# Kernel optimization log

Hardware: AMD Instinct MI355X
Metric: run time of the kernel (lower is better)

The kernel has to match this reference:

```python
import jax, jax.numpy as jnp
import numpy as np

B, T, S, A, H = 256, 256, 64, 16, 512  # batch, time, state_dim, action_dim, hypernet hidden


def setup_inputs() -> dict:
    key = jax.random.key(0)
    ks = jax.random.split(key, 12)
    x0 = jax.random.normal(ks[0], (B, S), dtype=jnp.float32)
    us = jax.random.normal(ks[1], (B, T, A), dtype=jnp.float32)
    # a_net: state_dim -> H -> S*S   (hypernetwork generating A(zx))
    Wa1 = jax.random.normal(ks[2], (S, H), dtype=jnp.float32) * 0.05
    ba1 = jax.random.normal(ks[3], (H,), dtype=jnp.float32) * 0.01
    Wa2 = jax.random.normal(ks[4], (H, S * S), dtype=jnp.float32) * 0.002  # small -> stable recurrence
    ba2 = jax.random.normal(ks[5], (S * S,), dtype=jnp.float32) * 0.002
    # b_net: action_dim -> H -> S*A  (hypernetwork generating B(zu))
    Wb1 = jax.random.normal(ks[6], (A, H), dtype=jnp.float32) * 0.05
    bb1 = jax.random.normal(ks[7], (H,), dtype=jnp.float32) * 0.01
    Wb2 = jax.random.normal(ks[8], (H, S * A), dtype=jnp.float32) * 0.02
    bb2 = jax.random.normal(ks[9], (S * A,), dtype=jnp.float32) * 0.02
    return {"x0": x0, "us": us, "Wa1": Wa1, "ba1": ba1, "Wa2": Wa2, "ba2": ba2,
            "Wb1": Wb1, "bb1": bb1, "Wb2": Wb2, "bb2": bb2}


def reference(x0, us, Wa1, ba1, Wa2, ba2, Wb1, bb1, Wb2, bb2):
    """HyperLinearSSM.rollout: x_{t+1} = A(x_t) @ x_t + B(u_t) @ u_t (zx=x, zu=u)."""
    def step(x, u):
        # hypernetwork-generated state matrix A(zx=x): [B, S, S]
        ha = jnp.tanh(x @ Wa1 + ba1)
        Amat = (ha @ Wa2 + ba2).reshape(-1, S, S)
        # hypernetwork-generated input matrix B(zu=u): [B, S, A]
        hb = jnp.tanh(u @ Wb1 + bb1)
        Bmat = (hb @ Wb2 + bb2).reshape(-1, S, A)
        x_next = jnp.einsum('bij,bj->bi', Amat, x) + jnp.einsum('bij,bj->bi', Bmat, u)
        return x_next, x_next

    us_t = jnp.transpose(us, (1, 0, 2))  # [T, B, A]
    _, xs = jax.lax.scan(step, x0, us_t)  # xs: [T, B, S]
    return jnp.transpose(xs, (1, 0, 2))   # [B, T, S]
```

## Files before the change

kernel.cpp:

```cpp
#include <hip/hip_runtime.h>

#define BSZ 256
#define TSZ 256
#define SSZ 64
#define ASZ 16
#define HSZ 512

typedef float f32x4 __attribute__((ext_vector_type(4)));
typedef short bf16x8 __attribute__((ext_vector_type(8)));
typedef unsigned short u16x8 __attribute__((ext_vector_type(8)));
typedef unsigned long long u64;
typedef unsigned short ushort_t;

#define XBUF_BYTES ((size_t)4 * BSZ * SSZ * sizeof(u64))
#define WT_ELEMS   ((size_t)4096 * 512)
#define WS_NEEDED  (XBUF_BYTES + 3 * WT_ELEMS * sizeof(ushort_t))


#define MF_X_OFF    0
#define MF_RED_OFF  4096
#define MF_HAH_OFF  4608
#define MF_HAM_OFF  (4608 + 16640)
#define MF_HAL_OFF  (21248 + 16640)
#define MF_WCH_OFF  (37888 + 16640)
#define MF_SMEM     (54528 + 2 * 3 * 16384)

#define NCH 16
#define HA_STR 20
#define X_OFF   0
#define HA_OFF  1024
#define W_OFF   (HA_OFF + HSZ * HA_STR)
#define RED_OFF (W_OFF + 3 * 32 * 256)
#define SMEM_FLOATS (RED_OFF + 512)
#define SMEM_BYTES  (SMEM_FLOATS * 4)

__device__ __forceinline__ void stage16(const void* gp, void* lp) {
    __builtin_amdgcn_global_load_lds(
        (const __attribute__((address_space(1))) void*)gp,
        (__attribute__((address_space(3))) void*)lp, 16, 0, 0);
}

__device__ __forceinline__ float wait_tag(const u64* p, unsigned tag) {
    u64 v = __hip_atomic_load(p, __ATOMIC_RELAXED, __HIP_MEMORY_SCOPE_AGENT);
    while ((unsigned)(v >> 32) != tag) {
        __builtin_amdgcn_s_sleep(1);
        v = __hip_atomic_load(p, __ATOMIC_RELAXED, __HIP_MEMORY_SCOPE_AGENT);
    }
    return __uint_as_float((unsigned)v);
}

__device__ __forceinline__ ushort_t f32_to_bf16(float f) {
    unsigned u = __float_as_uint(f);
    unsigned r = u + 0x7FFFu + ((u >> 16) & 1u);
    return (ushort_t)(r >> 16);
}
__device__ __forceinline__ float bf16_to_f32(ushort_t h) {
    return __uint_as_float((unsigned)h << 16);
}

__global__ __launch_bounds__(256) void wsplit_kernel(
    const float* __restrict__ Wa2,
    ushort_t* __restrict__ wth, ushort_t* __restrict__ wtm,
    ushort_t* __restrict__ wtl)
{
    __shared__ float tile[64][65];
    const int bc = blockIdx.x & 63;
    const int bh = blockIdx.x >> 6;
    const int c0 = bc * 64, h0 = bh * 64;
    const int tid = threadIdx.x;

    const int lr = tid >> 4, lc4 = (tid & 15) * 4;
    #pragma unroll
    for (int p = 0; p < 4; ++p) {
        const int h = p * 16 + lr;
        *(f32x4*)&tile[h][lc4] =
            *(const f32x4*)(Wa2 + (size_t)(h0 + h) * 4096 + c0 + lc4);
    }
    __syncthreads();

    const int col = tid >> 2, hb = (tid & 3) * 16;
    u16x8 H0, H1, M0, M1, L0, L1;
    #pragma unroll
    for (int q = 0; q < 16; ++q) {
        const float v = tile[hb + q][col];
        const ushort_t H = f32_to_bf16(v);
        const float r1 = v - bf16_to_f32(H);
        const ushort_t M = f32_to_bf16(r1);
        const ushort_t L = f32_to_bf16(r1 - bf16_to_f32(M));
        if (q < 8) { H0[q] = H; M0[q] = M; L0[q] = L; }
        else       { H1[q-8] = H; M1[q-8] = M; L1[q-8] = L; }
    }
    const int col_g = c0 + col;
    const int hbase = h0 + hb;
    const int kk    = hbase >> 5;
    const int sl0   = (hbase >> 3) & 3;
    const size_t atom0 = (((size_t)(col_g >> 5) * 16 + kk) * 4 + sl0) * 32
                       + (col_g & 31);
    const size_t atom1 = atom0 + 32;
    *(u16x8*)(wth + atom0 * 8) = H0;  *(u16x8*)(wth + atom1 * 8) = H1;
    *(u16x8*)(wtm + atom0 * 8) = M0;  *(u16x8*)(wtm + atom1 * 8) = M1;
    *(u16x8*)(wtl + atom0 * 8) = L0;  *(u16x8*)(wtl + atom1 * 8) = L1;
}

__global__ __launch_bounds__(256) void bu_kernel(
    const float* __restrict__ us,
    const float* __restrict__ Wb1, const float* __restrict__ bb1,
    const float* __restrict__ Wb2, const float* __restrict__ bb2,
    float* __restrict__ out)
{
    __shared__ float u_lds[16][16];
    __shared__ float hb_lds[16][HSZ + 4];

    const int tid = threadIdx.x;
    const long s0 = (long)blockIdx.x * 16;

    u_lds[tid >> 4][tid & 15] = us[s0 * ASZ + tid];
    __syncthreads();

    #pragma unroll
    for (int rep = 0; rep < 2; ++rep) {
        const int h = tid + rep * 256;
        float acc[16];
        const float b1 = bb1[h];
        #pragma unroll
        for (int s = 0; s < 16; ++s) acc[s] = b1;
        #pragma unroll
        for (int a = 0; a < ASZ; ++a) {
            const float w = Wb1[a * HSZ + h];
            #pragma unroll
            for (int s = 0; s < 16; ++s) acc[s] += u_lds[s][a] * w;
        }
        #pragma unroll
        for (int s = 0; s < 16; ++s) hb_lds[s][h] = tanhf(acc[s]);
    }
    __syncthreads();

    const int i  = tid & 63;
    const int sg = tid >> 6;

    float ur[4][ASZ];
    #pragma unroll
    for (int s4 = 0; s4 < 4; ++s4)
        #pragma unroll
        for (int a = 0; a < ASZ; ++a) ur[s4][a] = u_lds[sg * 4 + s4][a];

    float acc[4];
    {
        float wb[ASZ];
        const float4* bp = (const float4*)(bb2 + i * ASZ);
        #pragma unroll
        for (int q = 0; q < 4; ++q) {
            float4 v = bp[q];
            wb[q*4+0] = v.x; wb[q*4+1] = v.y; wb[q*4+2] = v.z; wb[q*4+3] = v.w;
        }
        #pragma unroll
        for (int s4 = 0; s4 < 4; ++s4) {
            float t = 0.f;
            #pragma unroll
            for (int a = 0; a < ASZ; ++a) t += wb[a] * ur[s4][a];
            acc[s4] = t;
        }
    }

    for (int h = 0; h < HSZ; ++h) {
        float w[ASZ];
        const float4* wp = (const float4*)(Wb2 + (size_t)h * (SSZ * ASZ) + i * ASZ);
        #pragma unroll
        for (int q = 0; q < 4; ++q) {
            float4 v = wp[q];
            w[q*4+0] = v.x; w[q*4+1] = v.y; w[q*4+2] = v.z; w[q*4+3] = v.w;
        }
        #pragma unroll
        for (int s4 = 0; s4 < 4; ++s4) {
            float t = 0.f;
            #pragma unroll
            for (int a = 0; a < ASZ; ++a) t += w[a] * ur[s4][a];
            acc[s4] += hb_lds[sg * 4 + s4][h] * t;
        }
    }

    #pragma unroll
    for (int s4 = 0; s4 < 4; ++s4)
        out[(s0 + sg * 4 + s4) * SSZ + i] = acc[s4];
}

__global__ __launch_bounds__(512, 1) void ssm_mfma(
    const float* __restrict__ x0,
    const float* __restrict__ Wa1, const float* __restrict__ ba1,
    const ushort_t* __restrict__ wth, const ushort_t* __restrict__ wtm,
    const ushort_t* __restrict__ wtl, const float* __restrict__ ba2,
    float* __restrict__ out, u64* __restrict__ xbuf)
{
    extern __shared__ char smem[];
    float* x_lds = (float*)(smem + MF_X_OFF);
    float* red   = (float*)(smem + MF_RED_OFF);
    char*  haH   = smem + MF_HAH_OFF;
    char*  haM   = smem + MF_HAM_OFF;
    char*  haL   = smem + MF_HAL_OFF;
    char*  wch   = smem + MF_WCH_OFF;

    const int tid  = threadIdx.x;
    const int lane = tid & 63;
    const int wv   = tid >> 6;
    const int l15  = lane & 15, lg = lane >> 4;
    const int bt = blockIdx.x >> 4, ct = blockIdx.x & 15;
    const long bbase = (long)bt * 16;

    const size_t wtile = (size_t)((ct * 8 + wv) * 16) * 1024 + (size_t)lane * 8;

    const float ba2v0 = ba2[ct * 256 + 32 * wv + l15];
    const float ba2v1 = ba2[ct * 256 + 32 * wv + 16 + l15];
    const int jt  = 32 * (wv & 1) + l15;
    const int s_e = l15, q_e = lg;

    const int abyte  = l15 * 1040 + lg * 16;
    const int b0byte = wv * 2048 + lg * 512 + l15 * 16;
    const int b1byte = b0byte + 256;

    for (int t = 0; t < TSZ; ++t) {
        {
            char* db = wch + wv * 2048;
            const ushort_t* gH = wth + wtile;
            const ushort_t* gM = wtm + wtile;
            const ushort_t* gL = wtl + wtile;
            stage16(gH, db);           stage16(gH + 512, db + 1024);
            stage16(gM, db + 16384);   stage16(gM + 512, db + 16384 + 1024);
            stage16(gL, db + 32768);   stage16(gL + 512, db + 32768 + 1024);
        }

        float bu_v = 0.f;
        if (wv == 0)
            bu_v = out[((bbase + s_e) * TSZ + t) * SSZ + (ct * 4 + q_e)];

        if (tid < 256) {
            const int sx = tid >> 4, jx = (tid & 15) * 4;
            float xv0, xv1, xv2, xv3;
            if (t > 0) {
                const u64* xs = xbuf + (size_t)((t - 1) & 3) * (BSZ * SSZ)
                              + (bbase + sx) * SSZ + jx;
                xv0 = wait_tag(xs + 0, (unsigned)t);
                xv1 = wait_tag(xs + 1, (unsigned)t);
                xv2 = wait_tag(xs + 2, (unsigned)t);
                xv3 = wait_tag(xs + 3, (unsigned)t);
            } else {
                const f32x4 x4 = *(const f32x4*)(x0 + (bbase + sx) * SSZ + jx);
                xv0 = x4.x; xv1 = x4.y; xv2 = x4.z; xv3 = x4.w;
            }
            x_lds[sx * SSZ + jx + 0] = xv0;
            x_lds[sx * SSZ + jx + 1] = xv1;
            x_lds[sx * SSZ + jx + 2] = xv2;
            x_lds[sx * SSZ + jx + 3] = xv3;
        }
        __syncthreads();

        {
            const int h0 = tid;
            float ar[16];
            const float b0 = ba1[h0];
            #pragma unroll
            for (int s = 0; s < 16; ++s) ar[s] = b0;
            #pragma unroll 4
            for (int jb = 0; jb < 16; ++jb) {
                float w0[4];
                #pragma unroll
                for (int q = 0; q < 4; ++q)
                    w0[q] = Wa1[(jb * 4 + q) * HSZ + h0];
                #pragma unroll
                for (int s = 0; s < 16; ++s) {
                    const f32x4 xr = *(const f32x4*)&x_lds[s * SSZ + jb * 4];
                    ar[s] += xr.x*w0[0] + xr.y*w0[1] + xr.z*w0[2] + xr.w*w0[3];
                }
            }
            #pragma unroll
            for (int s = 0; s < 16; ++s) {
                const float v = tanhf(ar[s]);
                const ushort_t H = f32_to_bf16(v);
                const float r1 = v - bf16_to_f32(H);
                const ushort_t M = f32_to_bf16(r1);
                const ushort_t L = f32_to_bf16(r1 - bf16_to_f32(M));
                ((ushort_t*)(haH + s * 1040))[h0] = H;
                ((ushort_t*)(haM + s * 1040))[h0] = M;
                ((ushort_t*)(haL + s * 1040))[h0] = L;
            }
        }
        __syncthreads();

        f32x4 acc0 = {0.f, 0.f, 0.f, 0.f};
        f32x4 acc1 = {0.f, 0.f, 0.f, 0.f};
        #pragma unroll
        for (int k = 0; k < 16; ++k) {
            if (k + 1 < 16) {
                char* db = wch + ((k + 1) & 1) * 49152 + wv * 2048;
                const ushort_t* gH = wth + wtile + (size_t)(k + 1) * 1024;
                const ushort_t* gM = wtm + wtile + (size_t)(k + 1) * 1024;
                const ushort_t* gL = wtl + wtile + (size_t)(k + 1) * 1024;
                stage16(gH, db);           stage16(gH + 512, db + 1024);
                stage16(gM, db + 16384);   stage16(gM + 512, db + 16384 + 1024);
                stage16(gL, db + 32768);   stage16(gL + 512, db + 32768 + 1024);
                asm volatile("s_waitcnt vmcnt(6)" ::: "memory");
            } else {
                asm volatile("s_waitcnt vmcnt(0)" ::: "memory");
            }
            __builtin_amdgcn_sched_barrier(0);

            const char* wb = wch + (k & 1) * 49152;
            const bf16x8 aH  = *(const bf16x8*)(haH + k * 64 + abyte);
            const bf16x8 aM  = *(const bf16x8*)(haM + k * 64 + abyte);
            const bf16x8 aL  = *(const bf16x8*)(haL + k * 64 + abyte);
            const bf16x8 b0H = *(const bf16x8*)(wb + b0byte);
            const bf16x8 b0M = *(const bf16x8*)(wb + 16384 + b0byte);
            const bf16x8 b0L = *(const bf16x8*)(wb + 32768 + b0byte);
            const bf16x8 b1H = *(const bf16x8*)(wb + b1byte);
            const bf16x8 b1M = *(const bf16x8*)(wb + 16384 + b1byte);
            const bf16x8 b1L = *(const bf16x8*)(wb + 32768 + b1byte);

            acc0 = __builtin_amdgcn_mfma_f32_16x16x32_bf16(aL, b0H, acc0, 0, 0, 0);
            acc0 = __builtin_amdgcn_mfma_f32_16x16x32_bf16(aM, b0M, acc0, 0, 0, 0);
            acc0 = __builtin_amdgcn_mfma_f32_16x16x32_bf16(aH, b0L, acc0, 0, 0, 0);
            acc0 = __builtin_amdgcn_mfma_f32_16x16x32_bf16(aM, b0H, acc0, 0, 0, 0);
            acc0 = __builtin_amdgcn_mfma_f32_16x16x32_bf16(aH, b0M, acc0, 0, 0, 0);
            acc0 = __builtin_amdgcn_mfma_f32_16x16x32_bf16(aH, b0H, acc0, 0, 0, 0);
            acc1 = __builtin_amdgcn_mfma_f32_16x16x32_bf16(aL, b1H, acc1, 0, 0, 0);
            acc1 = __builtin_amdgcn_mfma_f32_16x16x32_bf16(aM, b1M, acc1, 0, 0, 0);
            acc1 = __builtin_amdgcn_mfma_f32_16x16x32_bf16(aH, b1L, acc1, 0, 0, 0);
            acc1 = __builtin_amdgcn_mfma_f32_16x16x32_bf16(aM, b1H, acc1, 0, 0, 0);
            acc1 = __builtin_amdgcn_mfma_f32_16x16x32_bf16(aH, b1M, acc1, 0, 0, 0);
            acc1 = __builtin_amdgcn_mfma_f32_16x16x32_bf16(aH, b1H, acc1, 0, 0, 0);
        }

        float part[4];
        #pragma unroll
        for (int r = 0; r < 4; ++r) {
            const int s = lg * 4 + r;
            part[r] = (acc0[r] + ba2v0) * x_lds[s * SSZ + jt]
                    + (acc1[r] + ba2v1) * x_lds[s * SSZ + jt + 16];
            part[r] += __shfl_xor(part[r], 1);
            part[r] += __shfl_xor(part[r], 2);
            part[r] += __shfl_xor(part[r], 4);
            part[r] += __shfl_xor(part[r], 8);
        }
        if (l15 == 0) {
            #pragma unroll
            for (int r = 0; r < 4; ++r)
                red[wv * 16 + lg * 4 + r] = part[r];
        }
        __syncthreads();

        if (wv == 0) {
            const long b = bbase + s_e;
            const int  i = ct * 4 + q_e;
            const float xn = red[(2 * q_e) * 16 + s_e]
                           + red[(2 * q_e + 1) * 16 + s_e] + bu_v;
            out[(b * TSZ + t) * SSZ + i] = xn;
            const u64 w = ((u64)(unsigned)(t + 1) << 32)
                        | (u64)__float_as_uint(xn);
            __hip_atomic_store(xbuf + (size_t)(t & 3) * (BSZ * SSZ) + b * SSZ + i,
                               w, __ATOMIC_RELAXED, __HIP_MEMORY_SCOPE_AGENT);
        }
    }
}

__global__ __launch_bounds__(512, 1) void ssm_f32(
    const float* __restrict__ x0,
    const float* __restrict__ Wa1, const float* __restrict__ ba1,
    const float* __restrict__ Wa2, const float* __restrict__ ba2,
    float* __restrict__ out, u64* __restrict__ xbuf)
{
    extern __shared__ float smemf[];
    float* x_lds = smemf + X_OFF;
    float* ha_t  = smemf + HA_OFF;
    float* wchf  = smemf + W_OFF;
    float* redf  = smemf + RED_OFF;

    const int tid  = threadIdx.x;
    const int lane = tid & 63;
    const int wv   = tid >> 6;
    const int bt = blockIdx.x >> 4;
    const int ct = blockIdx.x & 15;
    const long bbase = (long)bt * 16;

    const int c0 = ct * 256 + lane * 4;
    const f32x4 ba2r = *(const f32x4*)(ba2 + c0);
    const int j0 = (lane & 15) * 4;
    const int s_e = lane & 15, il_e = lane >> 4;

    for (int t = 0; t < TSZ; ++t) {
        #pragma unroll
        for (int it = 0; it < 4; ++it)
            stage16(Wa2 + (size_t)(wv * 4 + it) * 4096 + c0,
                    wchf + (0 * 32 + wv * 4 + it) * 256);
        #pragma unroll
        for (int it = 0; it < 4; ++it)
            stage16(Wa2 + (size_t)(32 + wv * 4 + it) * 4096 + c0,
                    wchf + (1 * 32 + wv * 4 + it) * 256);

        float bu_v = 0.f;
        if (wv == 0)
            bu_v = out[((bbase + s_e) * TSZ + t) * SSZ + (ct * 4 + il_e)];

        if (tid < 256) {
            const int sx = tid >> 4, jx = (tid & 15) * 4;
            float xv0, xv1, xv2, xv3;
            if (t > 0) {
                const u64* xs = xbuf + (size_t)((t - 1) & 3) * (BSZ * SSZ)
                              + (bbase + sx) * SSZ + jx;
                xv0 = wait_tag(xs + 0, (unsigned)t);
                xv1 = wait_tag(xs + 1, (unsigned)t);
                xv2 = wait_tag(xs + 2, (unsigned)t);
                xv3 = wait_tag(xs + 3, (unsigned)t);
            } else {
                const f32x4 x4 = *(const f32x4*)(x0 + (bbase + sx) * SSZ + jx);
                xv0 = x4.x; xv1 = x4.y; xv2 = x4.z; xv3 = x4.w;
            }
            x_lds[sx * SSZ + jx + 0] = xv0;
            x_lds[sx * SSZ + jx + 1] = xv1;
            x_lds[sx * SSZ + jx + 2] = xv2;
            x_lds[sx * SSZ + jx + 3] = xv3;
        }
        __syncthreads();

        {
            const int h0 = tid;
            float ar[16];
            const float b0 = ba1[h0];
            #pragma unroll
            for (int s = 0; s < 16; ++s) ar[s] = b0;
            #pragma unroll 4
            for (int jb = 0; jb < 16; ++jb) {
                float w0[4];
                #pragma unroll
                for (int q = 0; q < 4; ++q)
                    w0[q] = Wa1[(jb * 4 + q) * HSZ + h0];
                #pragma unroll
                for (int s = 0; s < 16; ++s) {
                    const f32x4 xr = *(const f32x4*)&x_lds[s * SSZ + jb * 4];
                    ar[s] += xr.x*w0[0] + xr.y*w0[1] + xr.z*w0[2] + xr.w*w0[3];
                }
            }
            #pragma unroll
            for (int s = 0; s < 16; ++s) ar[s] = tanhf(ar[s]);
            #pragma unroll
            for (int q = 0; q < 4; ++q) {
                f32x4 v0;
                v0.x=ar[q*4+0]; v0.y=ar[q*4+1]; v0.z=ar[q*4+2]; v0.w=ar[q*4+3];
                *(f32x4*)&ha_t[h0 * HA_STR + q * 4] = v0;
            }
        }
        __syncthreads();

        f32x4 acc[16];
        {
            const f32x4 zero = {0.f, 0.f, 0.f, 0.f};
            const f32x4 ini = (wv == 0) ? ba2r : zero;
            #pragma unroll
            for (int s = 0; s < 16; ++s) acc[s] = ini;
        }
        for (int k = 0; k < NCH; ++k) {
            if (k + 2 < NCH) {
                #pragma unroll
                for (int it = 0; it < 4; ++it)
                    stage16(Wa2 + (size_t)((k + 2) * 32 + wv * 4 + it) * 4096 + c0,
                            wchf + (((k + 2) % 3) * 32 + wv * 4 + it) * 256);
                asm volatile("s_waitcnt vmcnt(8)" ::: "memory");
            } else if (k + 1 < NCH) {
                asm volatile("s_waitcnt vmcnt(4)" ::: "memory");
            } else {
                asm volatile("s_waitcnt vmcnt(0)" ::: "memory");
            }
            __builtin_amdgcn_sched_barrier(0);

            const float* wb = wchf + (k % 3) * 8192 + (wv * 4) * 256;
            const float* hb = ha_t + (size_t)(k * 32 + wv * 4) * HA_STR;
            #pragma unroll
            for (int rr = 0; rr < 4; ++rr) {
                const f32x4 w4 = *(const f32x4*)(wb + rr * 256 + lane * 4);
                const f32x4 h0 = *(const f32x4*)(hb + rr * HA_STR + 0);
                const f32x4 h1 = *(const f32x4*)(hb + rr * HA_STR + 4);
                const f32x4 h2 = *(const f32x4*)(hb + rr * HA_STR + 8);
                const f32x4 h3 = *(const f32x4*)(hb + rr * HA_STR + 12);
                acc[0]  += h0.x * w4; acc[1]  += h0.y * w4;
                acc[2]  += h0.z * w4; acc[3]  += h0.w * w4;
                acc[4]  += h1.x * w4; acc[5]  += h1.y * w4;
                acc[6]  += h1.z * w4; acc[7]  += h1.w * w4;
                acc[8]  += h2.x * w4; acc[9]  += h2.y * w4;
                acc[10] += h2.z * w4; acc[11] += h2.w * w4;
                acc[12] += h3.x * w4; acc[13] += h3.y * w4;
                acc[14] += h3.z * w4; acc[15] += h3.w * w4;
            }
        }

        float part[16];
        #pragma unroll
        for (int s = 0; s < 16; ++s) {
            const f32x4 xr = *(const f32x4*)&x_lds[s * SSZ + j0];
            part[s] = acc[s].x*xr.x + acc[s].y*xr.y + acc[s].z*xr.z + acc[s].w*xr.w;
        }
        #pragma unroll
        for (int s = 0; s < 16; ++s) {
            part[s] += __shfl_xor(part[s], 1);
            part[s] += __shfl_xor(part[s], 2);
            part[s] += __shfl_xor(part[s], 4);
            part[s] += __shfl_xor(part[s], 8);
        }
        if ((lane & 15) == 0) {
            const int il = lane >> 4;
            #pragma unroll
            for (int s = 0; s < 16; ++s)
                redf[(wv * 4 + il) * 16 + s] = part[s];
        }
        __syncthreads();

        if (wv == 0) {
            const long b = bbase + s_e;
            const int  i = ct * 4 + il_e;
            float r = 0.f;
            #pragma unroll
            for (int w8 = 0; w8 < 8; ++w8)
                r += redf[(w8 * 4 + il_e) * 16 + s_e];
            const float xn = r + bu_v;
            out[(b * TSZ + t) * SSZ + i] = xn;
            const u64 w = ((u64)(unsigned)(t + 1) << 32)
                        | (u64)__float_as_uint(xn);
            __hip_atomic_store(xbuf + (size_t)(t & 3) * (BSZ * SSZ) + b * SSZ + i,
                               w, __ATOMIC_RELAXED, __HIP_MEMORY_SCOPE_AGENT);
        }
    }
}

extern "C" void kernel_launch(void* const* d_in, const int* in_sizes, int n_in,
                              void* d_out, int out_size, void* d_ws, size_t ws_size,
                              hipStream_t stream) {
    const float* x0  = (const float*)d_in[0];
    const float* us  = (const float*)d_in[1];
    const float* Wa1 = (const float*)d_in[2];
    const float* ba1 = (const float*)d_in[3];
    const float* Wa2 = (const float*)d_in[4];
    const float* ba2 = (const float*)d_in[5];
    const float* Wb1 = (const float*)d_in[6];
    const float* bb1 = (const float*)d_in[7];
    const float* Wb2 = (const float*)d_in[8];
    const float* bb2 = (const float*)d_in[9];
    float* out = (float*)d_out;

    u64* xbuf = (u64*)d_ws;
    hipMemsetAsync(xbuf, 0, XBUF_BYTES, stream);

    hipLaunchKernelGGL(bu_kernel, dim3((BSZ * TSZ) / 16), dim3(256), 0, stream,
                       us, Wb1, bb1, Wb2, bb2, out);

    if (ws_size >= WS_NEEDED) {
        ushort_t* wth = (ushort_t*)((char*)d_ws + XBUF_BYTES);
        ushort_t* wtm = wth + WT_ELEMS;
        ushort_t* wtl = wtm + WT_ELEMS;
        hipLaunchKernelGGL(wsplit_kernel, dim3(512), dim3(256), 0, stream,
                           Wa2, wth, wtm, wtl);
        (void)hipFuncSetAttribute((const void*)ssm_mfma,
                                  hipFuncAttributeMaxDynamicSharedMemorySize, MF_SMEM);
        void* args[] = {(void*)&x0, (void*)&Wa1, (void*)&ba1,
                        (void*)&wth, (void*)&wtm, (void*)&wtl, (void*)&ba2,
                        (void*)&out, (void*)&xbuf};
        hipLaunchCooperativeKernel((const void*)ssm_mfma, dim3(256), dim3(512),
                                   args, MF_SMEM, stream);
    } else {
        (void)hipFuncSetAttribute((const void*)ssm_f32,
                                  hipFuncAttributeMaxDynamicSharedMemorySize, SMEM_BYTES);
        void* args[] = {(void*)&x0, (void*)&Wa1, (void*)&ba1,
                        (void*)&Wa2, (void*)&ba2, (void*)&out, (void*)&xbuf};
        hipLaunchCooperativeKernel((const void*)ssm_f32, dim3(256), dim3(512),
                                   args, SMEM_BYTES, stream);
    }
}
```

Before: 7.172 ms.

## Load hypernet weight tiles directly into registers with 3-deep prefetch

Replaces the global-to-LDS staging of the split-bf16 Wa2 tiles (double-buffered in shared memory, with explicit vmcnt waits) with direct global loads into VGPRs, prefetched two k-steps ahead in a 3-slot register ring. The tanh activation split buffers are also re-laid out in LDS so the MFMA A-operand reads match the new K ordering, and the LDS footprint shrinks. The aim is to remove LDS round-trips and waits on the weight stream. The cost is higher register pressure (18 bf16x8 vectors) and relying on the compiler to schedule the global-load latency.

```diff
diff --git a/kernel.cpp b/kernel.cpp
--- a/kernel.cpp
+++ b/kernel.cpp
@@ -20,10 +20,9 @@
 #define MF_X_OFF    0
 #define MF_RED_OFF  4096
 #define MF_HAH_OFF  4608
-#define MF_HAM_OFF  (4608 + 16640)
-#define MF_HAL_OFF  (21248 + 16640)
-#define MF_WCH_OFF  (37888 + 16640)
-#define MF_SMEM     (54528 + 2 * 3 * 16384)
+#define MF_HAM_OFF  (4608 + 18944)
+#define MF_HAL_OFF  (23552 + 18944)
+#define MF_SMEM     (42496 + 18944)
 
 #define NCH 16
 #define HA_STR 20
@@ -197,7 +196,6 @@
     char*  haH   = smem + MF_HAH_OFF;
     char*  haM   = smem + MF_HAM_OFF;
     char*  haL   = smem + MF_HAL_OFF;
-    char*  wch   = smem + MF_WCH_OFF;
 
     const int tid  = threadIdx.x;
     const int lane = tid & 63;
@@ -206,27 +204,34 @@
     const int bt = blockIdx.x >> 4, ct = blockIdx.x & 15;
     const long bbase = (long)bt * 16;
 
-    const size_t wtile = (size_t)((ct * 8 + wv) * 16) * 1024 + (size_t)lane * 8;
+    const size_t wtile = (size_t)((ct * 8 + wv) * 16) * 1024
+                       + (size_t)(lg * 256 + l15 * 8);
 
     const float ba2v0 = ba2[ct * 256 + 32 * wv + l15];
     const float ba2v1 = ba2[ct * 256 + 32 * wv + 16 + l15];
     const int jt  = 32 * (wv & 1) + l15;
     const int s_e = l15, q_e = lg;
 
-    const int abyte  = l15 * 1040 + lg * 16;
-    const int b0byte = wv * 2048 + lg * 512 + l15 * 16;
-    const int b1byte = b0byte + 256;
+    const int abyte = lg * 288 + l15 * 16;
+
+    const int kkh = tid >> 5, slh = (tid >> 3) & 3, eh = tid & 7;
+    const int hw_off = kkh * 1184 + slh * 288 + eh * 2;
+
+    #define LOAD6(dst, kk_) do {                                              \
+        const size_t b_ = wtile + (size_t)(kk_) * 1024;                       \
+        dst[0] = *(const bf16x8*)(wth + b_);                                  \
+        dst[1] = *(const bf16x8*)(wth + b_ + 128);                            \
+        dst[2] = *(const bf16x8*)(wtm + b_);                                  \
+        dst[3] = *(const bf16x8*)(wtm + b_ + 128);                            \
+        dst[4] = *(const bf16x8*)(wtl + b_);                                  \
+        dst[5] = *(const bf16x8*)(wtl + b_ + 128);                            \
+    } while (0)
 
     for (int t = 0; t < TSZ; ++t) {
-        {
-            char* db = wch + wv * 2048;
-            const ushort_t* gH = wth + wtile;
-            const ushort_t* gM = wtm + wtile;
-            const ushort_t* gL = wtl + wtile;
-            stage16(gH, db);           stage16(gH + 512, db + 1024);
-            stage16(gM, db + 16384);   stage16(gM + 512, db + 16384 + 1024);
-            stage16(gL, db + 32768);   stage16(gL + 512, db + 32768 + 1024);
-        }
+        bf16x8 f[3][6];
+        LOAD6(f[0], 0);
+        LOAD6(f[1], 1);
+        __builtin_amdgcn_sched_barrier(0);
 
         float bu_v = 0.f;
         if (wv == 0)
@@ -278,9 +283,9 @@
                 const float r1 = v - bf16_to_f32(H);
                 const ushort_t M = f32_to_bf16(r1);
                 const ushort_t L = f32_to_bf16(r1 - bf16_to_f32(M));
-                ((ushort_t*)(haH + s * 1040))[h0] = H;
-                ((ushort_t*)(haM + s * 1040))[h0] = M;
-                ((ushort_t*)(haL + s * 1040))[h0] = L;
+                *(ushort_t*)(haH + hw_off + s * 16) = H;
+                *(ushort_t*)(haM + hw_off + s * 16) = M;
+                *(ushort_t*)(haL + hw_off + s * 16) = L;
             }
         }
         __syncthreads();
@@ -289,30 +294,14 @@
         f32x4 acc1 = {0.f, 0.f, 0.f, 0.f};
         #pragma unroll
         for (int k = 0; k < 16; ++k) {
-            if (k + 1 < 16) {
-                char* db = wch + ((k + 1) & 1) * 49152 + wv * 2048;
-                const ushort_t* gH = wth + wtile + (size_t)(k + 1) * 1024;
-                const ushort_t* gM = wtm + wtile + (size_t)(k + 1) * 1024;
-                const ushort_t* gL = wtl + wtile + (size_t)(k + 1) * 1024;
-                stage16(gH, db);           stage16(gH + 512, db + 1024);
-                stage16(gM, db + 16384);   stage16(gM + 512, db + 16384 + 1024);
-                stage16(gL, db + 32768);   stage16(gL + 512, db + 32768 + 1024);
-                asm volatile("s_waitcnt vmcnt(6)" ::: "memory");
-            } else {
-                asm volatile("s_waitcnt vmcnt(0)" ::: "memory");
-            }
-            __builtin_amdgcn_sched_barrier(0);
-
-            const char* wb = wch + (k & 1) * 49152;
-            const bf16x8 aH  = *(const bf16x8*)(haH + k * 64 + abyte);
-            const bf16x8 aM  = *(const bf16x8*)(haM + k * 64 + abyte);
-            const bf16x8 aL  = *(const bf16x8*)(haL + k * 64 + abyte);
-            const bf16x8 b0H = *(const bf16x8*)(wb + b0byte);
-            const bf16x8 b0M = *(const bf16x8*)(wb + 16384 + b0byte);
-            const bf16x8 b0L = *(const bf16x8*)(wb + 32768 + b0byte);
-            const bf16x8 b1H = *(const bf16x8*)(wb + b1byte);
-            const bf16x8 b1M = *(const bf16x8*)(wb + 16384 + b1byte);
-            const bf16x8 b1L = *(const bf16x8*)(wb + 32768 + b1byte);
+            if (k + 2 < 16) LOAD6(f[(k + 2) % 3], k + 2);
+
+            const bf16x8 aH = *(const bf16x8*)(haH + k * 1184 + abyte);
+            const bf16x8 aM = *(const bf16x8*)(haM + k * 1184 + abyte);
+            const bf16x8 aL = *(const bf16x8*)(haL + k * 1184 + abyte);
+            const bf16x8 b0H = f[k % 3][0], b1H = f[k % 3][1];
+            const bf16x8 b0M = f[k % 3][2], b1M = f[k % 3][3];
+            const bf16x8 b0L = f[k % 3][4], b1L = f[k % 3][5];
 
             acc0 = __builtin_amdgcn_mfma_f32_16x16x32_bf16(aL, b0H, acc0, 0, 0, 0);
             acc0 = __builtin_amdgcn_mfma_f32_16x16x32_bf16(aM, b0M, acc0, 0, 0, 0);
@@ -358,6 +347,7 @@
                                w, __ATOMIC_RELAXED, __HIP_MEMORY_SCOPE_AGENT);
         }
     }
+    #undef LOAD6
 }
 
 __global__ __launch_bounds__(512, 1) void ssm_f32(
```

After: 9.498 ms. +32.4%, slower.
